# Kernel tuning notes

Hardware: AMD Instinct MI355X
Metric: run time of the kernel (lower is better)

Reference implementation:

```python
import jax, jax.numpy as jnp
import numpy as np


def setup_inputs() -> dict:
    key = jax.random.key(0)
    k1, k2 = jax.random.split(key)
    B, C, H, W = 4, 16, 48, 64
    ae = jax.random.normal(k1, (B, C, H, W), dtype=jnp.float32)
    # smoothness weights must be non-negative for an SPD system (as in practice,
    # where they come from a sigmoid/softplus head)
    wxwy = jax.random.uniform(k2, (B, 2, H, W), dtype=jnp.float32)
    return {"ae": ae, "wxwy": wxwy}


def _build_system(ae, wxwy):
    """Builds the normal-equation matrix L = I + Dx^T Wx Dx + Dy^T Wy Dy
    and rhs b = ae (unary residual with unit weight), matching the
    GridFactor unary/horizontal/vertical factor construction."""
    B, C, H, W = ae.shape
    HW = H * W
    wx = wxwy[:, 0]  # [B,H,W] horizontal weights, last column inactive
    wy = wxwy[:, 1]  # [B,H,W] vertical weights, last row inactive

    idx = jnp.arange(HW).reshape(H, W)
    ph = idx[:, :-1].ravel()   # horizontal factor: node (i,j)
    qh = idx[:, 1:].ravel()    # node (i,j+1)
    pv = idx[:-1, :].ravel()   # vertical factor: node (i,j)
    qv = idx[1:, :].ravel()    # node (i+1,j)
    wh = wx[:, :, :-1].reshape(B, -1)  # [B, H*(W-1)]
    wv = wy[:, :-1, :].reshape(B, -1)  # [B, (H-1)*W]

    # diagonal: unary weight 1 at every node + pairwise contributions
    diag = jnp.ones((B, HW), ae.dtype)
    diag = diag.at[:, ph].add(wh).at[:, qh].add(wh)
    diag = diag.at[:, pv].add(wv).at[:, qv].add(wv)

    L = jnp.zeros((B, HW, HW), ae.dtype)
    L = L.at[:, ph, qh].add(-wh).at[:, qh, ph].add(-wh)
    L = L.at[:, pv, qv].add(-wv).at[:, qv, pv].add(-wv)
    r = jnp.arange(HW)
    L = L.at[:, r, r].add(diag)

    # b = At(r) with residuals (ae, 0, 0) and unit unary weight -> b == ae
    b = ae.transpose(0, 2, 3, 1).reshape(B, HW, C)
    return L, b


def reference(ae, wxwy):
    B, C, H, W = ae.shape
    L, b = _build_system(ae, wxwy)
    x = jnp.linalg.solve(L, b)  # [B, HW, C]  (SPD system, exact solve)
    return x.reshape(B, H, W, C).transpose(0, 3, 1, 2)
```

## Files before the change

kernel.cpp:

```cpp
#include <hip/hip_runtime.h>

namespace {
constexpr int GH = 48;
constexpr int GW = 64;
constexpr int GHW = GH * GW;
constexpr int NT = 1024;
constexpr int NPT = GHW / NT;
constexpr int NITER = 18;
}

__global__ __launch_bounds__(NT)
void gridsmoother_cheb(const float* __restrict__ ae,
                       const float* __restrict__ wxwy,
                       float* __restrict__ out)
{
    const int bc = blockIdx.x;
    const int b  = bc >> 4;
    const int t  = threadIdx.x;

    const float* __restrict__ bvec = ae   + (size_t)bc * GHW;
    const float* __restrict__ gwx  = wxwy + (size_t)b * 2 * GHW;
    const float* __restrict__ gwy  = gwx + GHW;

    __shared__ float s_d[2][GHW];

    float x[NPT], r[NPT], d[NPT], dg[NPT];
    float wl[NPT], wrt[NPT], wu[NPT], wdn[NPT];
    int il[NPT], ir[NPT], iu[NPT], idn[NPT];

    constexpr float theta  = 5.0f;
    constexpr float delta  = 4.0f;
    constexpr float sigma1 = theta / delta;

    #pragma unroll
    for (int k = 0; k < NPT; ++k) {
        const int i  = t + k * NT;
        const int yy = i >> 6;
        const int xx = i & 63;
        il[k]  = (xx > 0)      ? i - 1  : i;
        ir[k]  = (xx < GW - 1) ? i + 1  : i;
        iu[k]  = (yy > 0)      ? i - GW : i;
        idn[k] = (yy < GH - 1) ? i + GW : i;
        wl[k]  = (xx > 0)      ? gwx[i - 1]  : 0.0f;
        wrt[k] = (xx < GW - 1) ? gwx[i]      : 0.0f;
        wu[k]  = (yy > 0)      ? gwy[i - GW] : 0.0f;
        wdn[k] = (yy < GH - 1) ? gwy[i]      : 0.0f;
        dg[k]  = 1.0f + wl[k] + wrt[k] + wu[k] + wdn[k];
        const float bvi = bvec[i];
        x[k] = 0.0f;
        r[k] = bvi;
        d[k] = bvi * (1.0f / theta);
        s_d[0][i] = d[k];
    }
    __syncthreads();

    float rho = 1.0f / sigma1;
    int cur = 0;

    #pragma unroll 1
    for (int it = 0; it < NITER; ++it) {
        const float* __restrict__ sd = s_d[cur];
        float ad[NPT];
        #pragma unroll
        for (int k = 0; k < NPT; ++k) {
            ad[k] = dg[k] * d[k]
                  - wl[k]  * sd[il[k]]  - wrt[k] * sd[ir[k]]
                  - wu[k]  * sd[iu[k]]  - wdn[k] * sd[idn[k]];
        }
        const float rho_new = 1.0f / (2.0f * sigma1 - rho);
        const float c1 = rho_new * rho;
        const float c2 = 2.0f * rho_new / delta;
        float* __restrict__ sn = s_d[cur ^ 1];
        #pragma unroll
        for (int k = 0; k < NPT; ++k) {
            x[k] += d[k];
            r[k] -= ad[k];
            d[k]  = c1 * d[k] + c2 * r[k];
            sn[t + k * NT] = d[k];
        }
        rho = rho_new;
        cur ^= 1;
        __syncthreads();
    }

    float* __restrict__ obase = out + (size_t)bc * GHW;
    #pragma unroll
    for (int k = 0; k < NPT; ++k) {
        obase[t + k * NT] = x[k];
    }
}

extern "C" void kernel_launch(void* const* d_in, const int* in_sizes, int n_in,
                              void* d_out, int out_size, void* d_ws, size_t ws_size,
                              hipStream_t stream) {
    const float* ae   = (const float*)d_in[0];
    const float* wxwy = (const float*)d_in[1];
    float* out = (float*)d_out;
    hipLaunchKernelGGL(gridsmoother_cheb, dim3(64), dim3(NT), 0, stream,
                       ae, wxwy, out);
}
```

Before: 63.54 us.

## Keep grid rows in registers per wave and exchange only halo rows via LDS

Each block now uses 4 wavefronts, and each one owns a contiguous band of 12 grid rows held in registers. Horizontal neighbours come from wave shuffles, vertical neighbours inside the band come from adjacent registers, and only the first and last rows of each band go through shared memory. This removes the full-grid LDS write and four gathered LDS reads per node on every iteration. The cost is fewer threads per block and lower parallelism, and each thread now works through a longer serial chain of 12 nodes.

```diff
diff --git a/kernel.cpp b/kernel.cpp
--- a/kernel.cpp
+++ b/kernel.cpp
@@ -1,11 +1,12 @@
 #include <hip/hip_runtime.h>
 
 namespace {
-constexpr int GH = 48;
-constexpr int GW = 64;
+constexpr int GH  = 48;
+constexpr int GW  = 64;
 constexpr int GHW = GH * GW;
-constexpr int NT = 1024;
-constexpr int NPT = GHW / NT;
+constexpr int NW  = 4;
+constexpr int NT  = NW * 64;
+constexpr int RPW = GH / NW;
 constexpr int NITER = 18;
 }
 
@@ -17,76 +18,83 @@
     const int bc = blockIdx.x;
     const int b  = bc >> 4;
     const int t  = threadIdx.x;
+    const int w  = t >> 6;
+    const int ln = t & 63;
+    const int r0 = w * RPW;
 
     const float* __restrict__ bvec = ae   + (size_t)bc * GHW;
     const float* __restrict__ gwx  = wxwy + (size_t)b * 2 * GHW;
     const float* __restrict__ gwy  = gwx + GHW;
 
-    __shared__ float s_d[2][GHW];
+    __shared__ float s_bnd[2][2][NW][GW];
 
-    float x[NPT], r[NPT], d[NPT], dg[NPT];
-    float wl[NPT], wrt[NPT], wu[NPT], wdn[NPT];
-    int il[NPT], ir[NPT], iu[NPT], idn[NPT];
+    float x[RPW], r[RPW], d[RPW], dg[RPW];
+    float wl[RPW], wrt[RPW], wu[RPW], wdn[RPW];
 
     constexpr float theta  = 5.0f;
     constexpr float delta  = 4.0f;
     constexpr float sigma1 = theta / delta;
 
     #pragma unroll
-    for (int k = 0; k < NPT; ++k) {
-        const int i  = t + k * NT;
-        const int yy = i >> 6;
-        const int xx = i & 63;
-        il[k]  = (xx > 0)      ? i - 1  : i;
-        ir[k]  = (xx < GW - 1) ? i + 1  : i;
-        iu[k]  = (yy > 0)      ? i - GW : i;
-        idn[k] = (yy < GH - 1) ? i + GW : i;
-        wl[k]  = (xx > 0)      ? gwx[i - 1]  : 0.0f;
-        wrt[k] = (xx < GW - 1) ? gwx[i]      : 0.0f;
-        wu[k]  = (yy > 0)      ? gwy[i - GW] : 0.0f;
-        wdn[k] = (yy < GH - 1) ? gwy[i]      : 0.0f;
-        dg[k]  = 1.0f + wl[k] + wrt[k] + wu[k] + wdn[k];
-        const float bvi = bvec[i];
-        x[k] = 0.0f;
-        r[k] = bvi;
-        d[k] = bvi * (1.0f / theta);
-        s_d[0][i] = d[k];
+    for (int j = 0; j < RPW; ++j) {
+        const int row = r0 + j;
+        const float wxv = gwx[row * GW + ln];
+        const float wyv = gwy[row * GW + ln];
+        wrt[j] = (ln < GW - 1) ? wxv : 0.0f;
+        const float wlv = __shfl_up(wxv, 1, 64);
+        wl[j]  = (ln > 0) ? wlv : 0.0f;
+        wdn[j] = (row < GH - 1) ? wyv : 0.0f;
+        wu[j]  = (row > 0) ? gwy[(row - 1) * GW + ln] : 0.0f;
+        dg[j]  = 1.0f + wl[j] + wrt[j] + wu[j] + wdn[j];
+        const float bv = bvec[row * GW + ln];
+        x[j] = 0.0f;
+        r[j] = bv;
+        d[j] = bv * (1.0f / theta);
     }
+    s_bnd[0][0][w][ln] = d[0];
+    s_bnd[0][1][w][ln] = d[RPW - 1];
     __syncthreads();
+
+    const int wm = (w > 0)      ? w - 1 : 0;
+    const int wp = (w < NW - 1) ? w + 1 : NW - 1;
 
     float rho = 1.0f / sigma1;
     int cur = 0;
 
     #pragma unroll 1
     for (int it = 0; it < NITER; ++it) {
-        const float* __restrict__ sd = s_d[cur];
-        float ad[NPT];
+        const float dup = s_bnd[cur][1][wm][ln];
+        const float ddn = s_bnd[cur][0][wp][ln];
+        float ad[RPW];
         #pragma unroll
-        for (int k = 0; k < NPT; ++k) {
-            ad[k] = dg[k] * d[k]
-                  - wl[k]  * sd[il[k]]  - wrt[k] * sd[ir[k]]
-                  - wu[k]  * sd[iu[k]]  - wdn[k] * sd[idn[k]];
+        for (int j = 0; j < RPW; ++j) {
+            const float sL = __shfl_up(d[j], 1, 64);
+            const float sR = __shfl_down(d[j], 1, 64);
+            const float up = (j == 0)       ? dup : d[j - 1];
+            const float dn = (j == RPW - 1) ? ddn : d[j + 1];
+            ad[j] = dg[j] * d[j] - wl[j] * sL - wrt[j] * sR
+                  - wu[j] * up - wdn[j] * dn;
         }
         const float rho_new = 1.0f / (2.0f * sigma1 - rho);
         const float c1 = rho_new * rho;
         const float c2 = 2.0f * rho_new / delta;
-        float* __restrict__ sn = s_d[cur ^ 1];
         #pragma unroll
-        for (int k = 0; k < NPT; ++k) {
-            x[k] += d[k];
-            r[k] -= ad[k];
-            d[k]  = c1 * d[k] + c2 * r[k];
-            sn[t + k * NT] = d[k];
+        for (int j = 0; j < RPW; ++j) {
+            x[j] += d[j];
+            r[j] -= ad[j];
+            d[j]  = c1 * d[j] + c2 * r[j];
         }
+        s_bnd[cur ^ 1][0][w][ln] = d[0];
+        s_bnd[cur ^ 1][1][w][ln] = d[RPW - 1];
         rho = rho_new;
         cur ^= 1;
         __syncthreads();
     }
 
-    float* __restrict__ obase = out + (size_t)bc * GHW;
+    float* __restrict__ ob = out + (size_t)bc * GHW;
     #pragma unroll
-    for (int k = 0; k < NPT; ++k) {
-        obase[t + k * NT] = x[k];
+    for (int j = 0; j < RPW; ++j) {
+        ob[(r0 + j) * GW + ln] = x[j];
     }
 }
 
```

After: 63.91 us. No clear change (+0.6%).
